# Performance work log

Measured on AMD Instinct MI355X. Metric: run time of the kernel, lower is better.

## Reference

```python
import jax, jax.numpy as jnp
import numpy as np

N_NODES = 50000
N_EDGES = 800000
D_IN, D_HID, D_OUT = 128, 96, 32


def _lin_params(key, d_in, d_out):
    k1, k2 = jax.random.split(key)
    bound = 1.0 / np.sqrt(d_in)
    W = jax.random.uniform(k1, (d_in, d_out), jnp.float32, -bound, bound)
    b = jax.random.uniform(k2, (d_out,), jnp.float32, -bound, bound)
    return W, b


def setup_inputs() -> dict:
    key = jax.random.key(0)
    ks = jax.random.split(key, 11)
    x = jax.random.normal(ks[0], (N_NODES, D_IN), jnp.float32)
    edge_index = jax.random.randint(ks[1], (2, N_EDGES), 0, N_NODES, jnp.int64)
    Wq1, bq1 = _lin_params(ks[2], D_IN, D_HID)
    Wk1, bk1 = _lin_params(ks[3], D_IN, D_HID)
    Wv1, bv1 = _lin_params(ks[4], D_IN, D_HID)
    Ws1, bs1 = _lin_params(ks[5], D_IN, D_HID)
    Wq2, bq2 = _lin_params(ks[6], D_HID, D_HID)
    Wk2, bk2 = _lin_params(ks[7], D_HID, D_HID)
    Wv2, bv2 = _lin_params(ks[8], D_HID, D_HID)
    Ws2, bs2 = _lin_params(ks[9], D_HID, D_HID)
    Wd, bd = _lin_params(ks[10], D_HID, D_OUT)
    return dict(x=x, edge_index=edge_index,
                Wq1=Wq1, bq1=bq1, Wk1=Wk1, bk1=bk1, Wv1=Wv1, bv1=bv1, Ws1=Ws1, bs1=bs1,
                Wq2=Wq2, bq2=bq2, Wk2=Wk2, bk2=bk2, Wv2=Wv2, bv2=bv2, Ws2=Ws2, bs2=bs2,
                Wd=Wd, bd=bd)


def transformer_conv(x, src, dst, Wq, bq, Wk, bk, Wv, bv, Ws, bs):
    # PyG TransformerConv, heads=1, concat=True, root_weight=True, edge_dim=None
    q = x @ Wq + bq  # [N, d]
    k = x @ Wk + bk
    v = x @ Wv + bv
    d = q.shape[-1]
    scale = 1.0 / np.sqrt(d).astype(np.float32)
    alpha = jnp.sum(q[dst] * k[src], axis=-1) * scale  # [E]
    # segment softmax over destination nodes
    m = jax.ops.segment_max(alpha, dst, num_segments=N_NODES)  # [N]
    e = jnp.exp(alpha - m[dst])
    s = jax.ops.segment_sum(e, dst, num_segments=N_NODES)
    w = e / (s[dst] + 1e-16)
    out = jax.ops.segment_sum(w[:, None] * v[src], dst, num_segments=N_NODES)  # [N, d]
    return out + x @ Ws + bs  # root/skip connection


def reference(x, edge_index,
              Wq1, bq1, Wk1, bk1, Wv1, bv1, Ws1, bs1,
              Wq2, bq2, Wk2, bk2, Wv2, bv2, Ws2, bs2,
              Wd, bd):
    src, dst = edge_index[0], edge_index[1]
    h = transformer_conv(x, src, dst, Wq1, bq1, Wk1, bk1, Wv1, bv1, Ws1, bs1)
    h = jax.nn.relu(h)
    h = transformer_conv(h, src, dst, Wq2, bq2, Wk2, bk2, Wv2, bv2, Ws2, bs2)
    return h @ Wd + bd
```

## Files before the change

kernel.cpp:

```cpp
#include <hip/hip_runtime.h>
#include <hip/hip_bf16.h>
#include <math.h>

#define NN_C 50000
#define NE_C 800000
#define NBKT 196
#define E_PER_BLK 4096
#define S1_BLOCKS 196
#define S2_CAP 8192

typedef short bf16x8 __attribute__((ext_vector_type(8)));
typedef float f32x4 __attribute__((ext_vector_type(4)));

struct U3 { unsigned int x, y, z; };

__device__ inline float blo(unsigned int u) { return __uint_as_float(u << 16); }
__device__ inline float bhi(unsigned int u) { return __uint_as_float(u & 0xffff0000u); }

__device__ inline unsigned short bf16rne(float f) {
    union { __hip_bfloat16 h; unsigned short u; } c;
    c.h = __float2bfloat16(f);
    return c.u;
}
__device__ inline unsigned int pk2(float a, float b) {
    return (unsigned int)bf16rne(a) | ((unsigned int)bf16rne(b) << 16);
}

__device__ inline int block_incl_scan(int v, int lane, int wid, int* ws)
{
    int x = v;
    #pragma unroll
    for (int off = 1; off < 64; off <<= 1) {
        int t = __shfl_up(x, off);
        if (lane >= off) x += t;
    }
    if (lane == 63) ws[wid] = x;
    __syncthreads();
    int woff = 0;
    #pragma unroll
    for (int w = 0; w < 4; ++w)
        if (w < wid) woff += ws[w];
    return woff + x;
}

template<bool AF32>
__global__ __launch_bounds__(256) void gemm_mfma(
    const void* __restrict__ Ap, const unsigned short* __restrict__ Wt,
    const float* __restrict__ bias,
    unsigned short* __restrict__ aggb, unsigned short* __restrict__ qsb,
    int M)
{
    __shared__ char lds[65536];
    char* sA = lds;
    char* sB = lds + 32768;
    const int tid = threadIdx.x;
    const int r0 = blockIdx.x * 128;
    const int c0 = blockIdx.y * 128;
    const char* Wb = (const char*)Wt + (size_t)c0 * 256;

    if (AF32) {
        const char* Asrc = (const char*)Ap;
        #pragma unroll
        for (int sct = 0; sct < 8; ++sct) {
            int o = (sct * 256 + tid) * 16;
            int r = o >> 8;
            int gr = r0 + r; if (gr > M - 1) gr = M - 1;
            const char* p = Asrc + (size_t)gr * 512 + (o & 255) * 2;
            float4 a = *reinterpret_cast<const float4*>(p);
            float4 b = *reinterpret_cast<const float4*>(p + 16);
            uint4 val;
            val.x = pk2(a.x, a.y); val.y = pk2(a.z, a.w);
            val.z = pk2(b.x, b.y); val.w = pk2(b.z, b.w);
            *reinterpret_cast<uint4*>(sA + (o ^ ((r & 7) << 4))) = val;
        }
    } else {
        const char* Asrc = (const char*)Ap;
        #pragma unroll
        for (int sct = 0; sct < 8; ++sct) {
            int o = (sct * 256 + tid) * 16;
            int r = o >> 8;
            int gr = r0 + r; if (gr > M - 1) gr = M - 1;
            uint4 val = *reinterpret_cast<const uint4*>(Asrc + (size_t)gr * 256 + (o & 255));
            *reinterpret_cast<uint4*>(sA + (o ^ ((r & 7) << 4))) = val;
        }
    }
    #pragma unroll
    for (int sct = 0; sct < 8; ++sct) {
        int o = (sct * 256 + tid) * 16;
        int r = o >> 8;
        uint4 val = *reinterpret_cast<const uint4*>(Wb + o);
        *reinterpret_cast<uint4*>(sB + (o ^ ((r & 7) << 4))) = val;
    }
    __syncthreads();

    const int lane = tid & 63, wid = tid >> 6;
    const int wm = wid >> 1, wn = wid & 1;
    const int qw = lane >> 4, c16 = lane & 15;

    f32x4 acc[4][4];
    #pragma unroll
    for (int a = 0; a < 4; ++a)
        #pragma unroll
        for (int b = 0; b < 4; ++b) acc[a][b] = (f32x4){0.f, 0.f, 0.f, 0.f};

    int aoff[4], boff[4];
    #pragma unroll
    for (int fm = 0; fm < 4; ++fm) {
        int r = wm * 64 + fm * 16 + c16;
        aoff[fm] = r * 256 + ((qw * 16) ^ ((r & 7) << 4));
    }
    #pragma unroll
    for (int fn = 0; fn < 4; ++fn) {
        int r = wn * 64 + fn * 16 + c16;
        boff[fn] = r * 256 + ((qw * 16) ^ ((r & 7) << 4));
    }

    #pragma unroll
    for (int ks = 0; ks < 4; ++ks) {
        const int kx = ks * 64;
        bf16x8 af[4], bfr[4];
        #pragma unroll
        for (int fm = 0; fm < 4; ++fm)
            af[fm] = *reinterpret_cast<const bf16x8*>(sA + (aoff[fm] ^ kx));
        #pragma unroll
        for (int fn = 0; fn < 4; ++fn)
            bfr[fn] = *reinterpret_cast<const bf16x8*>(sB + (boff[fn] ^ kx));
        #pragma unroll
        for (int fm = 0; fm < 4; ++fm)
            #pragma unroll
            for (int fn = 0; fn < 4; ++fn)
                acc[fm][fn] = __builtin_amdgcn_mfma_f32_16x16x32_bf16(
                    af[fm], bfr[fn], acc[fm][fn], 0, 0, 0);
    }

    #pragma unroll
    for (int fn = 0; fn < 4; ++fn) {
        int colbase = c0 + wn * 64 + fn * 16;
        int g = colbase / 96;
        unsigned short* obuf; int elem0;
        if (g == 0)      { obuf = qsb;  elem0 = colbase; }
        else if (g == 3) { obuf = qsb;  elem0 = colbase - 192; }
        else             { obuf = aggb; elem0 = colbase - 96; }
        float bcol = bias[colbase + c16];
        #pragma unroll
        for (int fm = 0; fm < 4; ++fm) {
            #pragma unroll
            for (int j = 0; j < 4; ++j) {
                int rg = r0 + wm * 64 + fm * 16 + qw * 4 + j;
                float o = acc[fm][fn][j] + bcol;
                float o2 = __shfl_xor(o, 1);
                if (!(lane & 1) && rg < M) {
                    *reinterpret_cast<unsigned int*>(
                        (char*)obuf + (size_t)rg * 384 + (size_t)(elem0 + c16) * 2) = pk2(o, o2);
                }
            }
        }
    }
}

__global__ __launch_bounds__(256) void setup_kernel(
    const float* __restrict__ w0a, const float* __restrict__ w1a,
    const float* __restrict__ w2a, const float* __restrict__ w3a,
    const float* __restrict__ b0a, const float* __restrict__ b1a,
    const float* __restrict__ b2a, const float* __restrict__ b3a,
    const float* __restrict__ w0b, const float* __restrict__ w1b,
    const float* __restrict__ w2b, const float* __restrict__ w3b,
    const float* __restrict__ b0b, const float* __restrict__ b1b,
    const float* __restrict__ b2b, const float* __restrict__ b3b,
    const int* __restrict__ dst,
    unsigned short* __restrict__ WtA, float* __restrict__ b4a,
    unsigned short* __restrict__ WtB, float* __restrict__ b4b,
    int* __restrict__ bucketCnt)
{
    __shared__ int hist[NBKT];
    const int tid = threadIdx.x;
    const int blk = blockIdx.x;
    if (blk < 384) {
        const bool L2w = blk >= 192;
        int idx = (L2w ? blk - 192 : blk) * 256 + tid;
        int n = idx >> 7, k = idx & 127;
        int g = n / 96, c = n - g * 96;
        const float* w; const float* bb;
        if (!L2w) {
            w = (g == 0) ? w0a : (g == 1) ? w1a : (g == 2) ? w2a : w3a;
            bb = (g == 0) ? b0a : (g == 1) ? b1a : (g == 2) ? b2a : b3a;
            WtA[idx] = bf16rne((k < 128) ? w[(size_t)k * 96 + c] : 0.f);
            if (k == 0) b4a[n] = bb[c];
        } else {
            w = (g == 0) ? w0b : (g == 1) ? w1b : (g == 2) ? w2b : w3b;
            bb = (g == 0) ? b0b : (g == 1) ? b1b : (g == 2) ? b2b : b3b;
            WtB[idx] = bf16rne((k < 96) ? w[(size_t)k * 96 + c] : 0.f);
            if (k == 0) b4b[n] = bb[c];
        }
    } else {
        const int hb = blk - 384;
        for (int t = tid; t < NBKT; t += 256) hist[t] = 0;
        __syncthreads();
        const int e0 = hb * E_PER_BLK;
        const int ne = min(E_PER_BLK, NE_C - e0);
        for (int j = tid; j < ne; j += 256)
            atomicAdd(&hist[((unsigned)dst[e0 + j]) >> 8], 1);
        __syncthreads();
        for (int t = tid; t < NBKT; t += 256)
            if (hist[t]) atomicAdd(&bucketCnt[t], hist[t]);
    }
}

__global__ __launch_bounds__(256) void scanb_kernel(
    const int* __restrict__ bucketCnt, int* __restrict__ bucketBase,
    int* __restrict__ gCur)
{
    __shared__ int ws[4];
    const int tid = threadIdx.x;
    int v = (tid < NBKT) ? bucketCnt[tid] : 0;
    int incl = block_incl_scan(v, tid & 63, tid >> 6, ws);
    int excl = incl - v;
    if (tid < NBKT) { bucketBase[tid] = excl; gCur[tid] = excl; }
    if (tid == NBKT - 1) bucketBase[NBKT] = incl;
}

__global__ __launch_bounds__(256) void stage1_kernel(
    const int* __restrict__ src, const int* __restrict__ dst,
    int* __restrict__ gCur, unsigned int* __restrict__ bktArr)
{
    __shared__ int hist[NBKT], loff[NBKT], lcur[NBKT], gbase[NBKT];
    __shared__ unsigned int bufRaw[E_PER_BLK];
    __shared__ unsigned int buf[E_PER_BLK];
    __shared__ int ws[4];
    const int tid = threadIdx.x;
    const int e0 = blockIdx.x * E_PER_BLK;
    const int ne = min(E_PER_BLK, NE_C - e0);

    for (int t = tid; t < NBKT; t += 256) hist[t] = 0;
    __syncthreads();
    for (int j = tid; j < ne; j += 256) {
        int d = dst[e0 + j], s = src[e0 + j];
        unsigned int pk = ((unsigned)d << 16) | (unsigned)s;
        bufRaw[j] = pk;
        atomicAdd(&hist[(unsigned)d >> 8], 1);
    }
    __syncthreads();
    {
        int v = (tid < NBKT) ? hist[tid] : 0;
        int incl = block_incl_scan(v, tid & 63, tid >> 6, ws);
        if (tid < NBKT) { loff[tid] = incl - v; lcur[tid] = incl - v; }
    }
    __syncthreads();
    for (int j = tid; j < ne; j += 256) {
        unsigned int pk = bufRaw[j];
        int p = atomicAdd(&lcur[pk >> 24], 1);
        buf[p] = pk;
    }
    __syncthreads();
    if (tid < NBKT && hist[tid] > 0) gbase[tid] = atomicAdd(&gCur[tid], hist[tid]);
    __syncthreads();
    for (int j = tid; j < ne; j += 256) {
        unsigned int pk = buf[j];
        int b = pk >> 24;
        bktArr[gbase[b] + (j - loff[b])] = pk;
    }
}

__global__ __launch_bounds__(256) void stage2_kernel(
    const unsigned int* __restrict__ bktArr, const int* __restrict__ bucketBase,
    int* __restrict__ csrb, int* __restrict__ row)
{
    __shared__ int ncnt[256], noff[256], ncur[256];
    __shared__ int outb[S2_CAP];
    __shared__ int ws[4];
    const int tid = threadIdx.x;
    const int b = blockIdx.x;
    const int base = bucketBase[b];
    const int cnt = bucketBase[b + 1] - base;

    ncnt[tid] = 0;
    __syncthreads();
    for (int j = tid; j < cnt; j += 256)
        atomicAdd(&ncnt[(bktArr[base + j] >> 16) & 255], 1);
    __syncthreads();
    {
        int v = ncnt[tid];
        int incl = block_incl_scan(v, tid & 63, tid >> 6, ws);
        noff[tid] = incl - v; ncur[tid] = incl - v;
    }
    __syncthreads();
    for (int j = tid; j < cnt; j += 256) {
        unsigned int pk = bktArr[base + j];
        int p = atomicAdd(&ncur[(pk >> 16) & 255], 1);
        if (p < S2_CAP) outb[p] = (int)(pk & 0xFFFFu) * 384;
    }
    __syncthreads();
    for (int j = tid; j < cnt && j < S2_CAP; j += 256) csrb[base + j] = outb[j];
    const int node0 = b * 256;
    if (node0 + tid < NN_C) row[node0 + tid] = base + noff[tid];
    if (b == 0 && tid == 0) row[NN_C] = NE_C;
}

template<int MODE>
__global__ __launch_bounds__(256) void aggregate_kernel(
    const unsigned short* __restrict__ aggb, const unsigned short* __restrict__ qsb,
    const int* __restrict__ row, const int* __restrict__ csrb,
    const float* __restrict__ Wd, const float* __restrict__ bd,
    void* __restrict__ outv, int nnodes)
{
    __shared__ float headL[MODE == 1 ? (96 * 32 + 32 + 4 * 96) : 1];
    const int tid  = threadIdx.x;
    const int wid  = tid >> 6;
    const int lane = tid & 63;
    const int l = lane & 15;
    const int q = lane >> 4;
    const int n = blockIdx.x * 4 + wid;

    if constexpr (MODE == 1) {
        #pragma unroll
        for (int t = 0; t < 12; ++t) headL[t * 256 + tid] = Wd[t * 256 + tid];
        if (tid < 32) headL[3072 + tid] = bd[tid];
        __syncthreads();
    }

    const float scale = 0.10206207261596577f;
    const char* AG = (const char*)aggb;
    const char* QS = (const char*)qsb;
    const size_t qrb = (size_t)n * 384;

    U3 qd = *(const U3*)(QS + qrb + 12 * l);
    const float q0 = blo(qd.x) * scale, q1 = bhi(qd.x) * scale;
    const float q2 = blo(qd.y) * scale, q3 = bhi(qd.y) * scale;
    const float q4 = blo(qd.z) * scale, q5 = bhi(qd.z) * scale;

    const char* AGk = AG + 12 * l;
    const char* AGv = AG + 192 + 12 * l;

    float s = 0.f, a0 = 0.f, a1 = 0.f, a2 = 0.f, a3 = 0.f, a4 = 0.f, a5 = 0.f;
    const int beg = row[n], end = row[n + 1];

    auto quad = [&](int i0) {
        const int base = csrb[i0 + q];
        U3 kd = *(const U3*)(AGk + base);
        U3 vd = *(const U3*)(AGv + base);
        float p = q0 * blo(kd.x) + q1 * bhi(kd.x) + q2 * blo(kd.y)
                + q3 * bhi(kd.y) + q4 * blo(kd.z) + q5 * bhi(kd.z);
        #pragma unroll
        for (int off = 1; off < 16; off <<= 1) p += __shfl_xor(p, off);
        float e = __expf(p);
        s  += e;
        a0 += e * blo(vd.x); a1 += e * bhi(vd.x);
        a2 += e * blo(vd.y); a3 += e * bhi(vd.y);
        a4 += e * blo(vd.z); a5 += e * bhi(vd.z);
    };

    int i = beg;
    for (; i + 8 <= end; i += 8) { quad(i); quad(i + 4); }
    for (; i + 4 <= end; i += 4) quad(i);
    if (i < end) {
        const int j = i + q;
        const int jc = (j < end) ? j : (end - 1);
        const int base = csrb[jc];
        U3 kd = *(const U3*)(AGk + base);
        U3 vd = *(const U3*)(AGv + base);
        float p = q0 * blo(kd.x) + q1 * bhi(kd.x) + q2 * blo(kd.y)
                + q3 * bhi(kd.y) + q4 * blo(kd.z) + q5 * bhi(kd.z);
        #pragma unroll
        for (int off = 1; off < 16; off <<= 1) p += __shfl_xor(p, off);
        float e = (j < end) ? __expf(p) : 0.f;
        s  += e;
        a0 += e * blo(vd.x); a1 += e * bhi(vd.x);
        a2 += e * blo(vd.y); a3 += e * bhi(vd.y);
        a4 += e * blo(vd.z); a5 += e * bhi(vd.z);
    }
    #pragma unroll
    for (int off = 16; off < 64; off <<= 1) {
        s  += __shfl_xor(s, off);
        a0 += __shfl_xor(a0, off); a1 += __shfl_xor(a1, off);
        a2 += __shfl_xor(a2, off); a3 += __shfl_xor(a3, off);
        a4 += __shfl_xor(a4, off); a5 += __shfl_xor(a5, off);
    }
    const float inv = 1.0f / (s + 1e-16f);

    U3 sd = *(const U3*)(QS + qrb + 192 + 12 * l);
    float o0 = a0 * inv + blo(sd.x), o1 = a1 * inv + bhi(sd.x);
    float o2 = a2 * inv + blo(sd.y), o3 = a3 * inv + bhi(sd.y);
    float o4 = a4 * inv + blo(sd.z), o5 = a5 * inv + bhi(sd.z);

    if constexpr (MODE == 0) {
        o0 = fmaxf(o0, 0.f); o1 = fmaxf(o1, 0.f); o2 = fmaxf(o2, 0.f);
        o3 = fmaxf(o3, 0.f); o4 = fmaxf(o4, 0.f); o5 = fmaxf(o5, 0.f);
        char* O = (char*)outv;
        const size_t ob = (size_t)n * 256;
        if (q < 3) {
            float u0 = (q == 0) ? o0 : (q == 1) ? o2 : o4;
            float u1 = (q == 0) ? o1 : (q == 1) ? o3 : o5;
            *(unsigned int*)(O + ob + 12 * l + 4 * q) = pk2(u0, u1);
        } else {
            *(unsigned int*)(O + ob + 192 + 4 * l) = 0u;
        }
    } else {
        float* oW = headL + 3104 + wid * 96;
        if (q == 0) {
            oW[6 * l + 0] = o0; oW[6 * l + 1] = o1; oW[6 * l + 2] = o2;
            oW[6 * l + 3] = o3; oW[6 * l + 4] = o4; oW[6 * l + 5] = o5;
        }
        const int c = lane & 31, h = lane >> 5;
        const int d0 = h * 48;
        float acc = 0.f;
        #pragma unroll
        for (int d = 0; d < 48; ++d)
            acc += oW[d0 + d] * headL[(d0 + d) * 32 + c];
        acc += __shfl_xor(acc, 32);
        if (lane < 32)
            ((float*)outv)[(size_t)n * 32 + c] = acc + headL[3072 + c];
    }
}

extern "C" void kernel_launch(void* const* d_in, const int* in_sizes, int n_in,
                              void* d_out, int out_size, void* d_ws, size_t ws_size,
                              hipStream_t stream)
{
    const int NN = NN_C, NE = NE_C;
    const float* x  = (const float*)d_in[0];
    const int*   ei = (const int*)d_in[1];
    const int* src = ei;
    const int* dst = ei + NE;

    const float* Wq1 = (const float*)d_in[2];  const float* bq1 = (const float*)d_in[3];
    const float* Wk1 = (const float*)d_in[4];  const float* bk1 = (const float*)d_in[5];
    const float* Wv1 = (const float*)d_in[6];  const float* bv1 = (const float*)d_in[7];
    const float* Ws1 = (const float*)d_in[8];  const float* bs1 = (const float*)d_in[9];
    const float* Wq2 = (const float*)d_in[10]; const float* bq2 = (const float*)d_in[11];
    const float* Wk2 = (const float*)d_in[12]; const float* bk2 = (const float*)d_in[13];
    const float* Wv2 = (const float*)d_in[14]; const float* bv2 = (const float*)d_in[15];
    const float* Ws2 = (const float*)d_in[16]; const float* bs2 = (const float*)d_in[17];
    const float* Wd  = (const float*)d_in[18]; const float* bd  = (const float*)d_in[19];

    char* base = (char*)d_ws;
    size_t off = 0;
    auto alloc = [&](size_t bytes) -> void* {
        void* p = base + off;
        off += (bytes + 255) & ~(size_t)255;
        return p;
    };
    unsigned short* aggb   = (unsigned short*)alloc((size_t)NN * 192 * 2);
    unsigned short* qsb    = (unsigned short*)alloc((size_t)NN * 192 * 2);
    unsigned short* hb16   = (unsigned short*)alloc((size_t)NN * 128 * 2);
    unsigned short* Wt4a   = (unsigned short*)alloc(384 * 128 * 2);
    unsigned short* Wt4b   = (unsigned short*)alloc(384 * 128 * 2);
    float*          b4a    = (float*)alloc(384 * 4);
    float*          b4b    = (float*)alloc(384 * 4);
    int*            bucketCnt  = (int*)alloc(NBKT * 4);
    int*            bucketBase = (int*)alloc((NBKT + 1) * 4);
    int*            gCur   = (int*)alloc(NBKT * 4);
    unsigned int*   bktArr = (unsigned int*)alloc((size_t)NE * 4);
    int*            csrb   = (int*)alloc((size_t)NE * 4);
    int*            rowp   = (int*)alloc((NN + 1) * 4);

    hipMemsetAsync(bucketCnt, 0, NBKT * sizeof(int), stream);
    setup_kernel<<<384 + S1_BLOCKS, 256, 0, stream>>>(
        Wq1, Wk1, Wv1, Ws1, bq1, bk1, bv1, bs1,
        Wq2, Wk2, Wv2, Ws2, bq2, bk2, bv2, bs2,
        dst, Wt4a, b4a, Wt4b, b4b, bucketCnt);
    scanb_kernel<<<1, 256, 0, stream>>>(bucketCnt, bucketBase, gCur);
    stage1_kernel<<<S1_BLOCKS, 256, 0, stream>>>(src, dst, gCur, bktArr);
    stage2_kernel<<<NBKT, 256, 0, stream>>>(bktArr, bucketBase, csrb, rowp);

    dim3 blk(256);
    dim3 gg((NN + 127) / 128, 3);
    const int aggGrid = NN / 4;

    gemm_mfma<true><<<gg, blk, 0, stream>>>(x, Wt4a, b4a, aggb, qsb, NN);
    aggregate_kernel<0><<<aggGrid, blk, 0, stream>>>(
        aggb, qsb, rowp, csrb, nullptr, nullptr, hb16, NN);

    gemm_mfma<false><<<gg, blk, 0, stream>>>(hb16, Wt4b, b4b, aggb, qsb, NN);
    aggregate_kernel<1><<<aggGrid, blk, 0, stream>>>(
        aggb, qsb, rowp, csrb, Wd, bd, d_out, NN);
}
```

Measured before the change: 285.3 us.

## Fuse layer-1 GEMM with CSR bucket scatter and shrink CSR indices to 16-bit

Merges the first-layer MFMA GEMM and the stage-1 edge bucketing into one launch, so the two independent jobs share the GPU. Per-block histograms now go to a partial array instead of global atomics, which removes the memset and the recount in stage 1, and stage 1 reads edges straight from global memory instead of staging them in LDS. CSR neighbor indices are stored as 16-bit node ids (times 384 at use), halving index traffic in aggregation, and the aggregation loop unrolls to 16 edges. Risks are LDS pressure in the fused kernel, a longer serial scan over 196 partials, and 16-bit ids relying on there being at most 65536 nodes.

```diff
diff --git a/kernel.cpp b/kernel.cpp
--- a/kernel.cpp
+++ b/kernel.cpp
@@ -8,6 +8,8 @@
 #define E_PER_BLK 4096
 #define S1_BLOCKS 196
 #define S2_CAP 8192
+#define GEMM_RB 391
+#define GEMM_BLOCKS (GEMM_RB * 3)
 
 typedef short bf16x8 __attribute__((ext_vector_type(8)));
 typedef float f32x4 __attribute__((ext_vector_type(4)));
@@ -44,18 +46,15 @@
 }
 
 template<bool AF32>
-__global__ __launch_bounds__(256) void gemm_mfma(
-    const void* __restrict__ Ap, const unsigned short* __restrict__ Wt,
+__device__ __forceinline__ void gemm_body(
+    char* lds, const void* __restrict__ Ap, const unsigned short* __restrict__ Wt,
     const float* __restrict__ bias,
     unsigned short* __restrict__ aggb, unsigned short* __restrict__ qsb,
-    int M)
-{
-    __shared__ char lds[65536];
+    int M, int r0, int c0)
+{
     char* sA = lds;
     char* sB = lds + 32768;
     const int tid = threadIdx.x;
-    const int r0 = blockIdx.x * 128;
-    const int c0 = blockIdx.y * 128;
     const char* Wb = (const char*)Wt + (size_t)c0 * 256;
 
     if (AF32) {
@@ -158,6 +157,16 @@
     }
 }
 
+template<bool AF32>
+__global__ __launch_bounds__(256) void gemm_mfma(
+    const void* __restrict__ Ap, const unsigned short* __restrict__ Wt,
+    const float* __restrict__ bias,
+    unsigned short* __restrict__ aggb, unsigned short* __restrict__ qsb, int M)
+{
+    __shared__ char lds[65536];
+    gemm_body<AF32>(lds, Ap, Wt, bias, aggb, qsb, M, blockIdx.x * 128, blockIdx.y * 128);
+}
+
 __global__ __launch_bounds__(256) void setup_kernel(
     const float* __restrict__ w0a, const float* __restrict__ w1a,
     const float* __restrict__ w2a, const float* __restrict__ w3a,
@@ -170,7 +179,7 @@
     const int* __restrict__ dst,
     unsigned short* __restrict__ WtA, float* __restrict__ b4a,
     unsigned short* __restrict__ WtB, float* __restrict__ b4b,
-    int* __restrict__ bucketCnt)
+    int* __restrict__ bucketPart)
 {
     __shared__ int hist[NBKT];
     const int tid = threadIdx.x;
@@ -202,43 +211,42 @@
             atomicAdd(&hist[((unsigned)dst[e0 + j]) >> 8], 1);
         __syncthreads();
         for (int t = tid; t < NBKT; t += 256)
-            if (hist[t]) atomicAdd(&bucketCnt[t], hist[t]);
+            bucketPart[hb * NBKT + t] = hist[t];
     }
 }
 
 __global__ __launch_bounds__(256) void scanb_kernel(
-    const int* __restrict__ bucketCnt, int* __restrict__ bucketBase,
+    const int* __restrict__ bucketPart, int* __restrict__ bucketBase,
     int* __restrict__ gCur)
 {
     __shared__ int ws[4];
     const int tid = threadIdx.x;
-    int v = (tid < NBKT) ? bucketCnt[tid] : 0;
+    int v = 0;
+    if (tid < NBKT)
+        for (int b = 0; b < S1_BLOCKS; ++b) v += bucketPart[b * NBKT + tid];
     int incl = block_incl_scan(v, tid & 63, tid >> 6, ws);
     int excl = incl - v;
     if (tid < NBKT) { bucketBase[tid] = excl; gCur[tid] = excl; }
     if (tid == NBKT - 1) bucketBase[NBKT] = incl;
 }
 
-__global__ __launch_bounds__(256) void stage1_kernel(
-    const int* __restrict__ src, const int* __restrict__ dst,
-    int* __restrict__ gCur, unsigned int* __restrict__ bktArr)
-{
-    __shared__ int hist[NBKT], loff[NBKT], lcur[NBKT], gbase[NBKT];
-    __shared__ unsigned int bufRaw[E_PER_BLK];
-    __shared__ unsigned int buf[E_PER_BLK];
-    __shared__ int ws[4];
+__device__ __forceinline__ void stage1_body(
+    char* ldsraw, const int* __restrict__ src, const int* __restrict__ dst,
+    const int* __restrict__ bucketPart, int* __restrict__ gCur,
+    unsigned int* __restrict__ bktArr, int blk)
+{
+    int* ip = (int*)ldsraw;
+    int* hist  = ip;
+    int* loff  = ip + 256;
+    int* lcur  = ip + 512;
+    int* gbase = ip + 768;
+    int* ws    = ip + 1024;
+    unsigned int* buf = (unsigned int*)(ip + 1056);
     const int tid = threadIdx.x;
-    const int e0 = blockIdx.x * E_PER_BLK;
+    const int e0 = blk * E_PER_BLK;
     const int ne = min(E_PER_BLK, NE_C - e0);
 
-    for (int t = tid; t < NBKT; t += 256) hist[t] = 0;
-    __syncthreads();
-    for (int j = tid; j < ne; j += 256) {
-        int d = dst[e0 + j], s = src[e0 + j];
-        unsigned int pk = ((unsigned)d << 16) | (unsigned)s;
-        bufRaw[j] = pk;
-        atomicAdd(&hist[(unsigned)d >> 8], 1);
-    }
+    if (tid < NBKT) hist[tid] = bucketPart[blk * NBKT + tid];
     __syncthreads();
     {
         int v = (tid < NBKT) ? hist[tid] : 0;
@@ -247,12 +255,16 @@
     }
     __syncthreads();
     for (int j = tid; j < ne; j += 256) {
-        unsigned int pk = bufRaw[j];
-        int p = atomicAdd(&lcur[pk >> 24], 1);
+        int d = dst[e0 + j], s = src[e0 + j];
+        unsigned int pk = ((unsigned)d << 16) | (unsigned)s;
+        int p = atomicAdd(&lcur[(unsigned)d >> 8], 1);
         buf[p] = pk;
     }
     __syncthreads();
-    if (tid < NBKT && hist[tid] > 0) gbase[tid] = atomicAdd(&gCur[tid], hist[tid]);
+    if (tid < NBKT) {
+        int h = hist[tid];
+        gbase[tid] = h ? atomicAdd(&gCur[tid], h) : 0;
+    }
     __syncthreads();
     for (int j = tid; j < ne; j += 256) {
         unsigned int pk = buf[j];
@@ -261,12 +273,31 @@
     }
 }
 
+__global__ __launch_bounds__(256) void fused1_kernel(
+    const float* __restrict__ x, const unsigned short* __restrict__ WtA,
+    const float* __restrict__ b4a,
+    unsigned short* __restrict__ aggb, unsigned short* __restrict__ qsb,
+    const int* __restrict__ src, const int* __restrict__ dst,
+    const int* __restrict__ bucketPart, int* __restrict__ gCur,
+    unsigned int* __restrict__ bktArr)
+{
+    __shared__ char lds[65536];
+    const int bx = blockIdx.x;
+    if (bx < GEMM_BLOCKS) {
+        int r0 = (bx % GEMM_RB) * 128;
+        int c0 = (bx / GEMM_RB) * 128;
+        gemm_body<true>(lds, x, WtA, b4a, aggb, qsb, NN_C, r0, c0);
+    } else {
+        stage1_body(lds, src, dst, bucketPart, gCur, bktArr, bx - GEMM_BLOCKS);
+    }
+}
+
 __global__ __launch_bounds__(256) void stage2_kernel(
     const unsigned int* __restrict__ bktArr, const int* __restrict__ bucketBase,
-    int* __restrict__ csrb, int* __restrict__ row)
+    unsigned short* __restrict__ csr16, int* __restrict__ row)
 {
     __shared__ int ncnt[256], noff[256], ncur[256];
-    __shared__ int outb[S2_CAP];
+    __shared__ unsigned short outb[S2_CAP];
     __shared__ int ws[4];
     const int tid = threadIdx.x;
     const int b = blockIdx.x;
@@ -287,10 +318,10 @@
     for (int j = tid; j < cnt; j += 256) {
         unsigned int pk = bktArr[base + j];
         int p = atomicAdd(&ncur[(pk >> 16) & 255], 1);
-        if (p < S2_CAP) outb[p] = (int)(pk & 0xFFFFu) * 384;
-    }
-    __syncthreads();
-    for (int j = tid; j < cnt && j < S2_CAP; j += 256) csrb[base + j] = outb[j];
+        if (p < S2_CAP) outb[p] = (unsigned short)(pk & 0xFFFFu);
+    }
+    __syncthreads();
+    for (int j = tid; j < cnt && j < S2_CAP; j += 256) csr16[base + j] = outb[j];
     const int node0 = b * 256;
     if (node0 + tid < NN_C) row[node0 + tid] = base + noff[tid];
     if (b == 0 && tid == 0) row[NN_C] = NE_C;
@@ -299,7 +330,7 @@
 template<int MODE>
 __global__ __launch_bounds__(256) void aggregate_kernel(
     const unsigned short* __restrict__ aggb, const unsigned short* __restrict__ qsb,
-    const int* __restrict__ row, const int* __restrict__ csrb,
+    const int* __restrict__ row, const unsigned short* __restrict__ csr16,
     const float* __restrict__ Wd, const float* __restrict__ bd,
     void* __restrict__ outv, int nnodes)
 {
@@ -335,7 +366,7 @@
     const int beg = row[n], end = row[n + 1];
 
     auto quad = [&](int i0) {
-        const int base = csrb[i0 + q];
+        const unsigned int base = (unsigned int)csr16[i0 + q] * 384u;
         U3 kd = *(const U3*)(AGk + base);
         U3 vd = *(const U3*)(AGv + base);
         float p = q0 * blo(kd.x) + q1 * bhi(kd.x) + q2 * blo(kd.y)
@@ -350,12 +381,12 @@
     };
 
     int i = beg;
-    for (; i + 8 <= end; i += 8) { quad(i); quad(i + 4); }
+    for (; i + 16 <= end; i += 16) { quad(i); quad(i + 4); quad(i + 8); quad(i + 12); }
     for (; i + 4 <= end; i += 4) quad(i);
     if (i < end) {
         const int j = i + q;
         const int jc = (j < end) ? j : (end - 1);
-        const int base = csrb[jc];
+        const unsigned int base = (unsigned int)csr16[jc] * 384u;
         U3 kd = *(const U3*)(AGk + base);
         U3 vd = *(const U3*)(AGv + base);
         float p = q0 * blo(kd.x) + q1 * bhi(kd.x) + q2 * blo(kd.y)
@@ -446,31 +477,29 @@
     unsigned short* Wt4b   = (unsigned short*)alloc(384 * 128 * 2);
     float*          b4a    = (float*)alloc(384 * 4);
     float*          b4b    = (float*)alloc(384 * 4);
-    int*            bucketCnt  = (int*)alloc(NBKT * 4);
+    int*            bucketPart = (int*)alloc((size_t)S1_BLOCKS * NBKT * 4);
     int*            bucketBase = (int*)alloc((NBKT + 1) * 4);
     int*            gCur   = (int*)alloc(NBKT * 4);
     unsigned int*   bktArr = (unsigned int*)alloc((size_t)NE * 4);
-    int*            csrb   = (int*)alloc((size_t)NE * 4);
+    unsigned short* csr16  = (unsigned short*)alloc((size_t)NE * 2);
     int*            rowp   = (int*)alloc((NN + 1) * 4);
 
-    hipMemsetAsync(bucketCnt, 0, NBKT * sizeof(int), stream);
     setup_kernel<<<384 + S1_BLOCKS, 256, 0, stream>>>(
         Wq1, Wk1, Wv1, Ws1, bq1, bk1, bv1, bs1,
         Wq2, Wk2, Wv2, Ws2, bq2, bk2, bv2, bs2,
-        dst, Wt4a, b4a, Wt4b, b4b, bucketCnt);
-    scanb_kernel<<<1, 256, 0, stream>>>(bucketCnt, bucketBase, gCur);
-    stage1_kernel<<<S1_BLOCKS, 256, 0, stream>>>(src, dst, gCur, bktArr);
-    stage2_kernel<<<NBKT, 256, 0, stream>>>(bktArr, bucketBase, csrb, rowp);
-
-    dim3 blk(256);
-    dim3 gg((NN + 127) / 128, 3);
+        dst, Wt4a, b4a, Wt4b, b4b, bucketPart);
+    scanb_kernel<<<1, 256, 0, stream>>>(bucketPart, bucketBase, gCur);
+
+    fused1_kernel<<<GEMM_BLOCKS + S1_BLOCKS, 256, 0, stream>>>(
+        x, Wt4a, b4a, aggb, qsb, src, dst, bucketPart, gCur, bktArr);
+    stage2_kernel<<<NBKT, 256, 0, stream>>>(bktArr, bucketBase, csr16, rowp);
+
     const int aggGrid = NN / 4;
-
-    gemm_mfma<true><<<gg, blk, 0, stream>>>(x, Wt4a, b4a, aggb, qsb, NN);
-    aggregate_kernel<0><<<aggGrid, blk, 0, stream>>>(
-        aggb, qsb, rowp, csrb, nullptr, nullptr, hb16, NN);
-
-    gemm_mfma<false><<<gg, blk, 0, stream>>>(hb16, Wt4b, b4b, aggb, qsb, NN);
-    aggregate_kernel<1><<<aggGrid, blk, 0, stream>>>(
-        aggb, qsb, rowp, csrb, Wd, bd, d_out, NN);
-}
+    aggregate_kernel<0><<<aggGrid, 256, 0, stream>>>(
+        aggb, qsb, rowp, csr16, nullptr, nullptr, hb16, NN);
+
+    dim3 gg(GEMM_RB, 3);
+    gemm_mfma<false><<<gg, 256, 0, stream>>>(hb16, Wt4b, b4b, aggb, qsb, NN);
+    aggregate_kernel<1><<<aggGrid, 256, 0, stream>>>(
+        aggb, qsb, rowp, csr16, Wd, bd, d_out, NN);
+}
```

Measured after the change: 294.9 us. +3.4%, slower.
